# Kernel optimization log

Measured on AMD Instinct MI355X. Metric: run time of the kernel, lower is better.

The kernel has to match this reference:

```python
import jax, jax.numpy as jnp
import numpy as np

N_NODES = 100000
N_EDGES = 1600000
F_IN = 64
HID = 128
N_CLASSES = 16
N_GRAPHS = 128


def _glorot(key, shape):
    fan_in = shape[1]
    bound = 1.0 / np.sqrt(fan_in)
    return jax.random.uniform(key, shape, jnp.float32, -bound, bound)


def setup_inputs() -> dict:
    key = jax.random.key(0)
    ks = jax.random.split(key, 12)
    x = jax.random.normal(ks[0], (N_NODES, F_IN), jnp.float32)
    edge_index = jax.random.randint(ks[1], (2, N_EDGES), 0, N_NODES, jnp.int64)
    batch = jnp.sort(jax.random.randint(ks[2], (N_NODES,), 0, N_GRAPHS, jnp.int64))
    # GraphConv l: out = lin_rel(sum_j x_j) + lin_root(x); lin_rel has bias, lin_root does not.
    W1_rel = _glorot(ks[3], (HID, F_IN)); b1 = jnp.zeros((HID,), jnp.float32)
    W1_root = _glorot(ks[4], (HID, F_IN))
    W2_rel = _glorot(ks[5], (HID, HID)); b2 = jnp.zeros((HID,), jnp.float32)
    W2_root = _glorot(ks[6], (HID, HID))
    W3_rel = _glorot(ks[7], (HID, HID)); b3 = jnp.zeros((HID,), jnp.float32)
    W3_root = _glorot(ks[8], (HID, HID))
    W_lin = _glorot(ks[9], (N_CLASSES, HID))
    b_lin = jnp.zeros((N_CLASSES,), jnp.float32)
    return {"x": x, "edge_index": edge_index, "batch": batch,
            "W1_rel": W1_rel, "b1": b1, "W1_root": W1_root,
            "W2_rel": W2_rel, "b2": b2, "W2_root": W2_root,
            "W3_rel": W3_rel, "b3": b3, "W3_root": W3_root,
            "W_lin": W_lin, "b_lin": b_lin}


def graph_conv(x, src, dst, W_rel, b_rel, W_root):
    # gather messages from source nodes, scatter-add at targets
    agg = jax.ops.segment_sum(x[src], dst, num_segments=N_NODES)  # [N, in]
    return agg @ W_rel.T + b_rel + x @ W_root.T


def reference(x, edge_index, batch, W1_rel, b1, W1_root, W2_rel, b2, W2_root,
              W3_rel, b3, W3_root, W_lin, b_lin):
    src, dst = edge_index[0], edge_index[1]
    h = jax.nn.relu(graph_conv(x, src, dst, W1_rel, b1, W1_root))
    h = jax.nn.relu(graph_conv(h, src, dst, W2_rel, b2, W2_root))
    h = graph_conv(h, src, dst, W3_rel, b3, W3_root)
    # global_mean_pool over batch ids
    sums = jax.ops.segment_sum(h, batch, num_segments=N_GRAPHS)  # [G, HID]
    counts = jax.ops.segment_sum(jnp.ones((h.shape[0],), h.dtype), batch,
                                 num_segments=N_GRAPHS)
    pooled = sums / jnp.maximum(counts, 1.0)[:, None]
    # dropout is identity in eval mode
    return pooled @ W_lin.T + b_lin
```

## Files before the change

kernel.cpp:

```cpp
#include <hip/hip_runtime.h>

#define N_NODES_C 100000
#define N_GRAPHS_C 128

typedef __attribute__((ext_vector_type(8))) __bf16 bf16x8;
typedef __attribute__((ext_vector_type(4))) float f32x4;

__device__ __forceinline__ f32x4 mfma16(bf16x8 a, bf16x8 b, f32x4 c) {
    return __builtin_amdgcn_mfma_f32_16x16x32_bf16(a, b, c, 0, 0, 0);
}

__device__ __forceinline__ void split2(float a, float b, unsigned& hi, unsigned& lo) {
    unsigned ua = __float_as_uint(a), ub = __float_as_uint(b);
    unsigned ha = ua & 0xFFFF0000u, hb = ub & 0xFFFF0000u;
    float la = a - __uint_as_float(ha), lb = b - __uint_as_float(hb);
    unsigned lpa = __float_as_uint(la) & 0xFFFF0000u;
    unsigned lpb = __float_as_uint(lb) & 0xFFFF0000u;
    hi = (ha >> 16) | hb;
    lo = (lpa >> 16) | lpb;
}

__device__ __forceinline__ void splitfrag(float4 v0, float4 v1, bf16x8& hi, bf16x8& lo) {
    unsigned h[4], l[4];
    split2(v0.x, v0.y, h[0], l[0]); split2(v0.z, v0.w, h[1], l[1]);
    split2(v1.x, v1.y, h[2], l[2]); split2(v1.z, v1.w, h[3], l[3]);
    uint4 uh = make_uint4(h[0], h[1], h[2], h[3]);
    uint4 ul = make_uint4(l[0], l[1], l[2], l[3]);
    hi = *(bf16x8*)&uh; lo = *(bf16x8*)&ul;
}

__global__ void hist_kernel(const int* __restrict__ ei, int E, int* __restrict__ deg) {
    int i = blockIdx.x * blockDim.x + threadIdx.x;
    if (i < E) atomicAdd(&deg[ei[E + i]], 1);
}

__global__ void scan1_kernel(const int* __restrict__ deg, int N,
                             int* __restrict__ tmp, int* __restrict__ bsum) {
    __shared__ int sh[512];
    int t = threadIdx.x;
    int i = blockIdx.x * 512 + t;
    int v = (i < N) ? deg[i] : 0;
    sh[t] = v;
    __syncthreads();
    for (int off = 1; off < 512; off <<= 1) {
        int add = (t >= off) ? sh[t - off] : 0;
        __syncthreads();
        sh[t] += add;
        __syncthreads();
    }
    if (i < N) tmp[i] = sh[t] - v;
    if (t == 511) bsum[blockIdx.x] = sh[511];
}

__global__ void scan2_kernel(int* bsum, int nb) {
    if (threadIdx.x == 0 && blockIdx.x == 0) {
        int run = 0;
        for (int j = 0; j < nb; ++j) { int v = bsum[j]; bsum[j] = run; run += v; }
    }
}

__global__ void scan3_kernel(const int* __restrict__ tmp, const int* __restrict__ bsum,
                             int N, int* __restrict__ rowp, int* __restrict__ rowpm) {
    int i = blockIdx.x * 512 + threadIdx.x;
    if (i < N) {
        int v = tmp[i] + bsum[blockIdx.x];
        rowp[i] = v;
        rowpm[i] = v;
    }
}

#define FILL_EPT 8
__global__ void fill_kernel(const int* __restrict__ ei, int E,
                            int* __restrict__ rowpm, int* __restrict__ csr) {
    int p = blockIdx.y;
    int base = blockIdx.x * 256 * FILL_EPT + threadIdx.x;
#pragma unroll
    for (int k = 0; k < FILL_EPT; ++k) {
        int i = base + k * 256;
        if (i < E) {
            int d = ei[E + i];
            if ((d >> 13) == p) {
                int pos = atomicAdd(&rowpm[d], 1);
                csr[pos] = ei[i];
            }
        }
    }
}

template <int FIN>
__global__ __launch_bounds__(256) void agg_kernel(const float* __restrict__ xin,
                                                  const int* __restrict__ rowp,
                                                  const int* __restrict__ degv,
                                                  const int* __restrict__ csrc,
                                                  float* __restrict__ aggout, int nNodes) {
    int wave = blockIdx.x * 4 + (threadIdx.x >> 6);
    int lane = threadIdx.x & 63;
    if (wave >= nNodes) return;
    int start = rowp[wave];
    int deg = degv[wave];
    const float4* x4 = (const float4*)xin;
    constexpr int EPW = (FIN == 128) ? 2 : 4;
    constexpr int RS = FIN / 4;
    const int grp = lane / RS;
    const int f4 = lane & (RS - 1);

    float4 acc[8];
#pragma unroll
    for (int q = 0; q < 8; ++q) acc[q] = make_float4(0.f, 0.f, 0.f, 0.f);

    for (int base = 0; base < deg; base += 64) {
        int cnt = min(64, deg - base);
        int sid = (lane < cnt) ? csrc[start + base + lane] : 0;
        int j = 0;
        for (; j + 8 * EPW <= cnt; j += 8 * EPW) {
            int n[8];
#pragma unroll
            for (int q = 0; q < 8; ++q) n[q] = __shfl(sid, j + q * EPW + grp);
            float4 v[8];
#pragma unroll
            for (int q = 0; q < 8; ++q) v[q] = x4[(size_t)n[q] * RS + f4];
#pragma unroll
            for (int q = 0; q < 8; ++q) {
                acc[q].x += v[q].x; acc[q].y += v[q].y;
                acc[q].z += v[q].z; acc[q].w += v[q].w;
            }
        }
        for (; j + EPW <= cnt; j += EPW) {
            int n0 = __shfl(sid, j + grp);
            float4 v = x4[(size_t)n0 * RS + f4];
            acc[0].x += v.x; acc[0].y += v.y; acc[0].z += v.z; acc[0].w += v.w;
        }
        for (; j < cnt; ++j) {
            int n0 = __shfl(sid, j);
            if (grp == 0) {
                float4 v = x4[(size_t)n0 * RS + f4];
                acc[0].x += v.x; acc[0].y += v.y; acc[0].z += v.z; acc[0].w += v.w;
            }
        }
    }
    float4 tot;
    tot.x = ((acc[0].x+acc[1].x)+(acc[2].x+acc[3].x)) + ((acc[4].x+acc[5].x)+(acc[6].x+acc[7].x));
    tot.y = ((acc[0].y+acc[1].y)+(acc[2].y+acc[3].y)) + ((acc[4].y+acc[5].y)+(acc[6].y+acc[7].y));
    tot.z = ((acc[0].z+acc[1].z)+(acc[2].z+acc[3].z)) + ((acc[4].z+acc[5].z)+(acc[6].z+acc[7].z));
    tot.w = ((acc[0].w+acc[1].w)+(acc[2].w+acc[3].w)) + ((acc[4].w+acc[5].w)+(acc[6].w+acc[7].w));
    if (FIN == 64) {
        tot.x += __shfl_xor(tot.x, 16); tot.y += __shfl_xor(tot.y, 16);
        tot.z += __shfl_xor(tot.z, 16); tot.w += __shfl_xor(tot.w, 16);
    }
    tot.x += __shfl_xor(tot.x, 32); tot.y += __shfl_xor(tot.y, 32);
    tot.z += __shfl_xor(tot.z, 32); tot.w += __shfl_xor(tot.w, 32);
    if (lane < RS)
        ((float4*)aggout)[(size_t)wave * RS + lane] = tot;
}

__global__ void wprep_kernel(const float* __restrict__ Wrel, const float* __restrict__ Wroot,
                             int KH, unsigned* __restrict__ img) {
    int cj = blockIdx.x;
    int l = threadIdx.x;
    int c = cj >> 3, j = cj & 7;
    int col = j * 16 + (l & 15);
    int k0 = c * 32 + (l >> 4) * 8;
    const float* src = (k0 < KH) ? Wrel : Wroot;
    int kk = (k0 < KH) ? k0 : k0 - KH;
    unsigned h[4], lo[4];
#pragma unroll
    for (int q = 0; q < 4; ++q) {
        float a = src[col * KH + kk + 2 * q];
        float b = src[col * KH + kk + 2 * q + 1];
        split2(a, b, h[q], lo[q]);
    }
    *(uint4*)&img[((size_t)cj * 2 + 0) * 256 + l * 4] = make_uint4(h[0], h[1], h[2], h[3]);
    *(uint4*)&img[((size_t)cj * 2 + 1) * 256 + l * 4] = make_uint4(lo[0], lo[1], lo[2], lo[3]);
}

template <int KTOT, bool RELU>
__global__ __launch_bounds__(256) void xform_kernel(
    const float* __restrict__ agg, const float* __restrict__ xin,
    const unsigned* __restrict__ wimg, const float* __restrict__ bias,
    float* __restrict__ hout, int nNodes)
{
    constexpr int KH = KTOT / 2;
    constexpr int NC = KTOT / 32;
    const int t = threadIdx.x;
    const int lane = t & 63, wv = t >> 6;
    const int r15 = lane & 15, hi4 = lane >> 4;
    const int nb0 = blockIdx.x * 128;
    const int row0 = nb0 + wv * 32 + r15;
    const int row1 = row0 + 16;
    const bool v0 = row0 < nNodes, v1 = row1 < nNodes;
    const float4 z4 = make_float4(0.f, 0.f, 0.f, 0.f);

    f32x4 acc[2][8];
#pragma unroll
    for (int g = 0; g < 2; ++g)
#pragma unroll
        for (int j = 0; j < 8; ++j) acc[g][j] = (f32x4){0.f, 0.f, 0.f, 0.f};
    float bj[8];
#pragma unroll
    for (int j = 0; j < 8; ++j) bj[j] = bias[j * 16 + r15];

#pragma unroll 1
    for (int c = 0; c < NC; ++c) {
        const float* srcA = (c * 32 < KH) ? agg : xin;
        const int ko = ((c * 32 < KH) ? (c * 32) : (c * 32 - KH)) + hi4 * 8;
        const float* p0 = &srcA[(size_t)row0 * KH + ko];
        const float* p1 = &srcA[(size_t)row1 * KH + ko];
        float4 a00 = v0 ? *(const float4*)p0 : z4;
        float4 a01 = v0 ? *(const float4*)(p0 + 4) : z4;
        float4 a10 = v1 ? *(const float4*)p1 : z4;
        float4 a11 = v1 ? *(const float4*)(p1 + 4) : z4;
        bf16x8 ah0, al0, ah1, al1;
        splitfrag(a00, a01, ah0, al0);
        splitfrag(a10, a11, ah1, al1);
        const unsigned* wc = wimg + (size_t)c * 4096;
#pragma unroll
        for (int j = 0; j < 8; ++j) {
            bf16x8 bh = *(const bf16x8*)&wc[(j * 2 + 0) * 256 + lane * 4];
            bf16x8 bl = *(const bf16x8*)&wc[(j * 2 + 1) * 256 + lane * 4];
            acc[0][j] = mfma16(ah0, bh, acc[0][j]);
            acc[1][j] = mfma16(ah1, bh, acc[1][j]);
            acc[0][j] = mfma16(ah0, bl, acc[0][j]);
            acc[1][j] = mfma16(ah1, bl, acc[1][j]);
            acc[0][j] = mfma16(al0, bh, acc[0][j]);
            acc[1][j] = mfma16(al1, bh, acc[1][j]);
        }
    }

#pragma unroll
    for (int g2 = 0; g2 < 2; ++g2) {
#pragma unroll
        for (int r = 0; r < 4; ++r) {
            int node = nb0 + wv * 32 + g2 * 16 + hi4 * 4 + r;
            if (node >= nNodes) continue;
            float* orow = &hout[(size_t)node * 128];
#pragma unroll
            for (int j = 0; j < 8; ++j) {
                float v = acc[g2][j][r] + bj[j];
                if (RELU) v = fmaxf(v, 0.f);
                orow[j * 16 + r15] = v;
            }
        }
    }
}

__global__ void bounds_kernel(const int* __restrict__ batch, int N, int* __restrict__ gstart) {
    int g = blockIdx.x * blockDim.x + threadIdx.x;
    if (g > N_GRAPHS_C) return;
    int lo = 0, hi = N;
    while (lo < hi) {
        int mid = (lo + hi) >> 1;
        if (batch[mid] < g) lo = mid + 1; else hi = mid;
    }
    gstart[g] = lo;
}

__global__ __launch_bounds__(256) void pool2_kernel(const float* __restrict__ h,
                                                    const int* __restrict__ gstart,
                                                    float* __restrict__ pooled) {
    int g = blockIdx.x;
    int f4 = threadIdx.x & 31;
    int sub = threadIdx.x >> 5;
    int s = gstart[g], e = gstart[g + 1];
    const float4* h4 = (const float4*)h;
    float4 acc = make_float4(0.f, 0.f, 0.f, 0.f);
    for (int n = s + sub; n < e; n += 8) {
        float4 v = h4[(size_t)n * 32 + f4];
        acc.x += v.x; acc.y += v.y; acc.z += v.z; acc.w += v.w;
    }
    __shared__ float4 sh[8][33];
    sh[sub][f4] = acc;
    __syncthreads();
    if (sub == 0) {
        float4 tot = acc;
#pragma unroll
        for (int q = 1; q < 8; ++q) {
            float4 v = sh[q][f4];
            tot.x += v.x; tot.y += v.y; tot.z += v.z; tot.w += v.w;
        }
        float inv = 1.0f / fmaxf((float)(e - s), 1.0f);
        tot.x *= inv; tot.y *= inv; tot.z *= inv; tot.w *= inv;
        ((float4*)pooled)[g * 32 + f4] = tot;
    }
}

__global__ void final_kernel(const float* __restrict__ pooled,
                             const float* __restrict__ Wlin, const float* __restrict__ blin,
                             float* __restrict__ out) {
    int idx = blockIdx.x * blockDim.x + threadIdx.x;
    int g = idx >> 4, c = idx & 15;
    float s = 0.f;
    for (int k = 0; k < 128; ++k) s += pooled[g * 128 + k] * Wlin[c * 128 + k];
    out[idx] = s + blin[c];
}

extern "C" void kernel_launch(void* const* d_in, const int* in_sizes, int n_in,
                              void* d_out, int out_size, void* d_ws, size_t ws_size,
                              hipStream_t stream) {
    const float* x      = (const float*)d_in[0];
    const int*   ei     = (const int*)d_in[1];
    const int*   batch  = (const int*)d_in[2];
    const float* W1_rel = (const float*)d_in[3];
    const float* b1     = (const float*)d_in[4];
    const float* W1_root= (const float*)d_in[5];
    const float* W2_rel = (const float*)d_in[6];
    const float* b2     = (const float*)d_in[7];
    const float* W2_root= (const float*)d_in[8];
    const float* W3_rel = (const float*)d_in[9];
    const float* b3     = (const float*)d_in[10];
    const float* W3_root= (const float*)d_in[11];
    const float* W_lin  = (const float*)d_in[12];
    const float* b_lin  = (const float*)d_in[13];
    float* out = (float*)d_out;

    const int N = in_sizes[2];
    const int E = in_sizes[1] / 2;
    const int nb = (N + 511) / 512;

    char* base = (char*)d_ws;
    size_t off = 0;
    auto carve = [&](size_t bytes) -> void* {
        void* p = base + off;
        off = (off + bytes + 255) & ~(size_t)255;
        return p;
    };
    int*      deg    = (int*)carve((size_t)N * 4);
    int*      tmp    = (int*)carve((size_t)N * 4);
    int*      bsum   = (int*)carve(1024);
    int*      rowp   = (int*)carve((size_t)(N + 1) * 4);
    int*      rowpm  = (int*)carve((size_t)N * 4);
    int*      csr    = (int*)carve((size_t)E * 4);
    float*    aggbuf = (float*)carve((size_t)N * 128 * 4);
    float*    hA     = (float*)carve((size_t)N * 128 * 4);
    float*    hB     = (float*)carve((size_t)N * 128 * 4);
    float*    pooled = (float*)carve((size_t)N_GRAPHS_C * 128 * 4);
    int*      gstart = (int*)carve((size_t)(N_GRAPHS_C + 1) * 4);
    unsigned* wimg1  = (unsigned*)carve((size_t)4 * 4096 * 4);
    unsigned* wimg2  = (unsigned*)carve((size_t)8 * 4096 * 4);
    unsigned* wimg3  = (unsigned*)carve((size_t)8 * 4096 * 4);
    (void)ws_size;

    hipMemsetAsync(deg, 0, (size_t)N * 4, stream);

    wprep_kernel<<<32, 64, 0, stream>>>(W1_rel, W1_root, 64, wimg1);
    wprep_kernel<<<64, 64, 0, stream>>>(W2_rel, W2_root, 128, wimg2);
    wprep_kernel<<<64, 64, 0, stream>>>(W3_rel, W3_root, 128, wimg3);

    hist_kernel<<<(E + 255) / 256, 256, 0, stream>>>(ei, E, deg);
    scan1_kernel<<<nb, 512, 0, stream>>>(deg, N, tmp, bsum);
    scan2_kernel<<<1, 64, 0, stream>>>(bsum, nb);
    scan3_kernel<<<nb, 512, 0, stream>>>(tmp, bsum, N, rowp, rowpm);
    const int npass = (N + 8191) >> 13;
    fill_kernel<<<dim3((E + 256 * FILL_EPT - 1) / (256 * FILL_EPT), npass), 256, 0, stream>>>(
        ei, E, rowpm, csr);

    bounds_kernel<<<1, 192, 0, stream>>>(batch, N, gstart);

    const int aggGrid = (N + 3) / 4;
    const int xGrid = (N + 127) / 128;

    agg_kernel<64><<<aggGrid, 256, 0, stream>>>(x, rowp, deg, csr, aggbuf, N);
    xform_kernel<128, true><<<xGrid, 256, 0, stream>>>(aggbuf, x, wimg1, b1, hA, N);

    agg_kernel<128><<<aggGrid, 256, 0, stream>>>(hA, rowp, deg, csr, aggbuf, N);
    xform_kernel<256, true><<<xGrid, 256, 0, stream>>>(aggbuf, hA, wimg2, b2, hB, N);

    agg_kernel<128><<<aggGrid, 256, 0, stream>>>(hB, rowp, deg, csr, aggbuf, N);
    xform_kernel<256, false><<<xGrid, 256, 0, stream>>>(aggbuf, hB, wimg3, b3, hA, N);

    pool2_kernel<<<N_GRAPHS_C, 256, 0, stream>>>(hA, gstart, pooled);
    final_kernel<<<8, 256, 0, stream>>>(pooled, W_lin, b_lin, out);
}
```

Before: 802.4 us.

## Partition histogram by destination range, parallelize block-sum scan, unify aggregation tail

The degree histogram now uses the same destination-range partitioned grid as the CSR fill, so each pass's atomics land in an 8192-node window that stays cache-resident. The single-threaded block-sum scan becomes a 512-thread shared-memory scan. The aggregation kernel's scalar tail loops are folded into the main 8-wide gather loop using clamped indices and predicated accumulation, which removes serial tail iterations at the cost of some redundant loads. The histogram reads the edge list once per pass, which multiplies its read traffic.

Result: faster. 776.1 us (-3.3%).

```diff
diff --git a/kernel.cpp b/kernel.cpp
--- a/kernel.cpp
+++ b/kernel.cpp
@@ -29,9 +29,19 @@
     hi = *(bf16x8*)&uh; lo = *(bf16x8*)&ul;
 }
 
+#define FILL_EPT 8
+
 __global__ void hist_kernel(const int* __restrict__ ei, int E, int* __restrict__ deg) {
-    int i = blockIdx.x * blockDim.x + threadIdx.x;
-    if (i < E) atomicAdd(&deg[ei[E + i]], 1);
+    int p = blockIdx.y;
+    int base = blockIdx.x * 256 * FILL_EPT + threadIdx.x;
+#pragma unroll
+    for (int k = 0; k < FILL_EPT; ++k) {
+        int i = base + k * 256;
+        if (i < E) {
+            int d = ei[E + i];
+            if ((d >> 13) == p) atomicAdd(&deg[d], 1);
+        }
+    }
 }
 
 __global__ void scan1_kernel(const int* __restrict__ deg, int N,
@@ -53,10 +63,18 @@
 }
 
 __global__ void scan2_kernel(int* bsum, int nb) {
-    if (threadIdx.x == 0 && blockIdx.x == 0) {
-        int run = 0;
-        for (int j = 0; j < nb; ++j) { int v = bsum[j]; bsum[j] = run; run += v; }
-    }
+    __shared__ int sh[512];
+    int t = threadIdx.x;
+    int v = (t < nb) ? bsum[t] : 0;
+    sh[t] = v;
+    __syncthreads();
+    for (int off = 1; off < 512; off <<= 1) {
+        int add = (t >= off) ? sh[t - off] : 0;
+        __syncthreads();
+        sh[t] += add;
+        __syncthreads();
+    }
+    if (t < nb) bsum[t] = sh[t] - v;
 }
 
 __global__ void scan3_kernel(const int* __restrict__ tmp, const int* __restrict__ bsum,
@@ -69,7 +87,6 @@
     }
 }
 
-#define FILL_EPT 8
 __global__ void fill_kernel(const int* __restrict__ ei, int E,
                             int* __restrict__ rowpm, int* __restrict__ csr) {
     int p = blockIdx.y;
@@ -111,30 +128,23 @@
     for (int base = 0; base < deg; base += 64) {
         int cnt = min(64, deg - base);
         int sid = (lane < cnt) ? csrc[start + base + lane] : 0;
-        int j = 0;
-        for (; j + 8 * EPW <= cnt; j += 8 * EPW) {
+        for (int j = 0; j < cnt; j += 8 * EPW) {
+            int rem = cnt - j;
             int n[8];
 #pragma unroll
-            for (int q = 0; q < 8; ++q) n[q] = __shfl(sid, j + q * EPW + grp);
+            for (int q = 0; q < 8; ++q) {
+                int e = q * EPW + grp;
+                n[q] = __shfl(sid, j + min(e, rem - 1));
+            }
             float4 v[8];
 #pragma unroll
             for (int q = 0; q < 8; ++q) v[q] = x4[(size_t)n[q] * RS + f4];
 #pragma unroll
             for (int q = 0; q < 8; ++q) {
-                acc[q].x += v[q].x; acc[q].y += v[q].y;
-                acc[q].z += v[q].z; acc[q].w += v[q].w;
-            }
-        }
-        for (; j + EPW <= cnt; j += EPW) {
-            int n0 = __shfl(sid, j + grp);
-            float4 v = x4[(size_t)n0 * RS + f4];
-            acc[0].x += v.x; acc[0].y += v.y; acc[0].z += v.z; acc[0].w += v.w;
-        }
-        for (; j < cnt; ++j) {
-            int n0 = __shfl(sid, j);
-            if (grp == 0) {
-                float4 v = x4[(size_t)n0 * RS + f4];
-                acc[0].x += v.x; acc[0].y += v.y; acc[0].z += v.z; acc[0].w += v.w;
+                if (q * EPW + grp < rem) {
+                    acc[q].x += v[q].x; acc[q].y += v[q].y;
+                    acc[q].z += v[q].z; acc[q].w += v[q].w;
+                }
             }
         }
     }
@@ -325,7 +335,7 @@
     };
     int*      deg    = (int*)carve((size_t)N * 4);
     int*      tmp    = (int*)carve((size_t)N * 4);
-    int*      bsum   = (int*)carve(1024);
+    int*      bsum   = (int*)carve(2048);
     int*      rowp   = (int*)carve((size_t)(N + 1) * 4);
     int*      rowpm  = (int*)carve((size_t)N * 4);
     int*      csr    = (int*)carve((size_t)E * 4);
@@ -345,13 +355,13 @@
     wprep_kernel<<<64, 64, 0, stream>>>(W2_rel, W2_root, 128, wimg2);
     wprep_kernel<<<64, 64, 0, stream>>>(W3_rel, W3_root, 128, wimg3);
 
-    hist_kernel<<<(E + 255) / 256, 256, 0, stream>>>(ei, E, deg);
+    const int npass = (N + 8191) >> 13;
+    const int fillGx = (E + 256 * FILL_EPT - 1) / (256 * FILL_EPT);
+    hist_kernel<<<dim3(fillGx, npass), 256, 0, stream>>>(ei, E, deg);
     scan1_kernel<<<nb, 512, 0, stream>>>(deg, N, tmp, bsum);
-    scan2_kernel<<<1, 64, 0, stream>>>(bsum, nb);
+    scan2_kernel<<<1, 512, 0, stream>>>(bsum, nb);
     scan3_kernel<<<nb, 512, 0, stream>>>(tmp, bsum, N, rowp, rowpm);
-    const int npass = (N + 8191) >> 13;
-    fill_kernel<<<dim3((E + 256 * FILL_EPT - 1) / (256 * FILL_EPT), npass), 256, 0, stream>>>(
-        ei, E, rowpm, csr);
+    fill_kernel<<<dim3(fillGx, npass), 256, 0, stream>>>(ei, E, rowpm, csr);
 
     bounds_kernel<<<1, 192, 0, stream>>>(batch, N, gstart);
 
```
